# Optimization experiments

Measured on AMD Instinct MI355X. Metric: run time of the kernel, lower is better.

Reference implementation:

```python
import jax, jax.numpy as jnp
import numpy as np

B, T, D = 8, 1024, 768
N_HEAD = 12
HEAD_DIM = D // N_HEAD


def setup_inputs() -> dict:
    key = jax.random.key(0)
    k1, k2, k3, k4, k5 = jax.random.split(key, 5)
    x = jax.random.normal(k1, (B, T, D), dtype=jnp.float32)
    # c_attn: Linear(D, 3D); c_proj: Linear(D, D). Stored as (in, out) for x @ W.
    s_attn = 1.0 / np.sqrt(D)
    W_attn = jax.random.uniform(k2, (D, 3 * D), dtype=jnp.float32, minval=-s_attn, maxval=s_attn)
    b_attn = jax.random.uniform(k3, (3 * D,), dtype=jnp.float32, minval=-s_attn, maxval=s_attn)
    W_proj = jax.random.uniform(k4, (D, D), dtype=jnp.float32, minval=-s_attn, maxval=s_attn)
    b_proj = jax.random.uniform(k5, (D,), dtype=jnp.float32, minval=-s_attn, maxval=s_attn)
    return {"x": x, "W_attn": W_attn, "b_attn": b_attn, "W_proj": W_proj, "b_proj": b_proj}


def reference(x, W_attn, b_attn, W_proj, b_proj):
    Bs, Ts, Ds = x.shape
    qkv = x @ W_attn + b_attn  # [B, T, 3D]
    Q, K, V = jnp.split(qkv, 3, axis=2)
    # [B, H, T, hd]
    Q = Q.reshape(Bs, Ts, N_HEAD, HEAD_DIM).transpose(0, 2, 1, 3)
    K = K.reshape(Bs, Ts, N_HEAD, HEAD_DIM).transpose(0, 2, 1, 3)
    V = V.reshape(Bs, Ts, N_HEAD, HEAD_DIM).transpose(0, 2, 1, 3)
    scale = HEAD_DIM ** (-0.5)
    scores = jnp.einsum('bhqd,bhkd->bhqk', Q, K) * scale  # [B, H, T, T]
    causal = jnp.tril(jnp.ones((Ts, Ts), dtype=bool))
    scores = jnp.where(causal[None, None, :, :], scores, -jnp.inf)
    probs = jax.nn.softmax(scores, axis=-1)
    attn = jnp.einsum('bhqk,bhkd->bhqd', probs, V)  # [B, H, T, hd]
    attn = attn.transpose(0, 2, 1, 3).reshape(Bs, Ts, Ds)
    return attn @ W_proj + b_proj
```

## Files before the change

kernel.cpp:

```cpp
#include <hip/hip_runtime.h>
#include <hip/hip_bf16.h>

#define B_ 8
#define T_ 1024
#define D_ 768
#define NH 12
#define HD 64

typedef __bf16 bf16x8 __attribute__((ext_vector_type(8)));
typedef __bf16 bf16x4 __attribute__((ext_vector_type(4)));
typedef float f32x4 __attribute__((ext_vector_type(4)));
typedef short s16x4 __attribute__((ext_vector_type(4)));

__device__ __forceinline__ float fast_exp2(float x) {
  return __builtin_amdgcn_exp2f(x);
}

__device__ __forceinline__ f32x4 mfma32(bf16x8 a, bf16x8 b, f32x4 c) {
  return __builtin_amdgcn_mfma_f32_16x16x32_bf16(a, b, c, 0, 0, 0);
}

__device__ __forceinline__ f32x4 mfma16(bf16x4 a, bf16x4 b, f32x4 c) {
  union U { bf16x4 h; s16x4 s; };
  U ua; ua.h = a;
  U ub; ub.h = b;
  return __builtin_amdgcn_mfma_f32_16x16x16bf16_1k(ua.s, ub.s, c, 0, 0, 0);
}

__device__ __forceinline__ void gload_lds16(const void* g, void* l) {
  __builtin_amdgcn_global_load_lds((const __attribute__((address_space(1))) unsigned int*)g,
                                   (__attribute__((address_space(3))) unsigned int*)l, 16, 0, 0);
}

__global__ void xconv_kernel(const float* __restrict__ x, __bf16* __restrict__ xb, int n8) {
  int i = blockIdx.x * 256 + threadIdx.x;
  if (i >= n8) return;
  const float4* xf = (const float4*)x;
  float4 a = xf[i * 2], b = xf[i * 2 + 1];
  bf16x8 v;
  v[0] = (__bf16)a.x; v[1] = (__bf16)a.y; v[2] = (__bf16)a.z; v[3] = (__bf16)a.w;
  v[4] = (__bf16)b.x; v[5] = (__bf16)b.y; v[6] = (__bf16)b.z; v[7] = (__bf16)b.w;
  *(bf16x8*)&xb[(size_t)i * 8] = v;
}

__global__ void wtrans_kernel(const float* __restrict__ W, __bf16* __restrict__ WT, int K, int N) {
  __shared__ float tile[32][33];
  int t = threadIdx.x, col = t & 31, r0 = t >> 5;
  int n0 = blockIdx.x * 32, k0 = blockIdx.y * 32;
#pragma unroll
  for (int p = 0; p < 4; p++) {
    int r = r0 + p * 8;
    tile[r][col] = W[(size_t)(k0 + r) * N + n0 + col];
  }
  __syncthreads();
#pragma unroll
  for (int p = 0; p < 4; p++) {
    int r = r0 + p * 8;
    WT[(size_t)(n0 + r) * K + k0 + col] = (__bf16)tile[col][r];
  }
}

template <int EPI>
__global__ __launch_bounds__(256) void gemm_kernel(const __bf16* __restrict__ A,
                                                   const __bf16* __restrict__ BT,
                                                   const float* __restrict__ bias,
                                                   void* __restrict__ Cout,
                                                   __bf16* __restrict__ VT,
                                                   int M, int N, int K, int nbx) {
  __shared__ __align__(16) __bf16 Asm[2][128 * 64];
  __shared__ __align__(16) __bf16 Bsm[2][128 * 64];
  int tid = threadIdx.x;
  int wave = tid >> 6, lane = tid & 63, g = lane >> 4, l15 = lane & 15;
  int wr = wave >> 1, wc = wave & 1;

  int wg = blockIdx.x;
  int cpx = gridDim.x >> 3;
  int wg2 = (wg & 7) * cpx + (wg >> 3);
  int bx = wg2 % nbx, by = wg2 / nbx;
  int m0 = by * 128, n0 = bx * 128;

  int srow = tid >> 3;
  int cc = (tid & 7) ^ ((tid >> 3) & 7);
  const __bf16* Ag = A + (size_t)(m0 + srow) * K + cc * 8;
  const __bf16* Bg = BT + (size_t)(n0 + srow) * K + cc * 8;

  auto stage = [&](int kt, int bf) {
#pragma unroll
    for (int i = 0; i < 4; i++) {
      gload_lds16(Ag + (size_t)(i * 32) * K + kt * 64, &Asm[bf][wave * 512 + i * 2048]);
      gload_lds16(Bg + (size_t)(i * 32) * K + kt * 64, &Bsm[bf][wave * 512 + i * 2048]);
    }
  };

  f32x4 zz = {0.0f, 0.0f, 0.0f, 0.0f};
  f32x4 acc[4][4];
#pragma unroll
  for (int m = 0; m < 4; m++)
#pragma unroll
    for (int n = 0; n < 4; n++) acc[m][n] = zz;

  int nk = K >> 6;
  int swr = l15 & 7;

  stage(0, 0);

  int cur = 0;
  for (int kt = 0; kt < nk; kt++) {
    if (kt + 1 < nk) {
      stage(kt + 1, cur ^ 1);
      asm volatile("s_waitcnt vmcnt(8)" ::: "memory");
    } else {
      asm volatile("s_waitcnt vmcnt(0)" ::: "memory");
    }
    __builtin_amdgcn_s_barrier();
#pragma unroll
    for (int ks = 0; ks < 2; ks++) {
      bf16x8 af[4], bfr[4];
#pragma unroll
      for (int m = 0; m < 4; m++) {
        int row = wr * 64 + m * 16 + l15;
        af[m] = *(const bf16x8*)&Asm[cur][row * 64 + ((ks * 4 + g) ^ swr) * 8];
      }
#pragma unroll
      for (int n = 0; n < 4; n++) {
        int row = wc * 64 + n * 16 + l15;
        bfr[n] = *(const bf16x8*)&Bsm[cur][row * 64 + ((ks * 4 + g) ^ swr) * 8];
      }
#pragma unroll
      for (int m = 0; m < 4; m++)
#pragma unroll
        for (int n = 0; n < 4; n++)
          acc[m][n] = __builtin_amdgcn_mfma_f32_16x16x32_bf16(af[m], bfr[n], acc[m][n], 0, 0, 0);
    }
    asm volatile("" ::: "memory");
    __builtin_amdgcn_s_barrier();
    cur ^= 1;
  }
#pragma unroll
  for (int n = 0; n < 4; n++) {
    int gcol = n0 + wc * 64 + n * 16 + l15;
    float bv = bias[gcol];
#pragma unroll
    for (int m = 0; m < 4; m++) {
      int grow0 = m0 + wr * 64 + m * 16 + g * 4;
      float v0 = acc[m][n][0] + bv, v1 = acc[m][n][1] + bv;
      float v2 = acc[m][n][2] + bv, v3 = acc[m][n][3] + bv;
      if (EPI == 1) {
        float* C = (float*)Cout;
        C[(size_t)(grow0 + 0) * N + gcol] = v0;
        C[(size_t)(grow0 + 1) * N + gcol] = v1;
        C[(size_t)(grow0 + 2) * N + gcol] = v2;
        C[(size_t)(grow0 + 3) * N + gcol] = v3;
      } else if (gcol < 2 * D_) {
        __bf16* C = (__bf16*)Cout;
        C[(size_t)(grow0 + 0) * N + gcol] = (__bf16)v0;
        C[(size_t)(grow0 + 1) * N + gcol] = (__bf16)v1;
        C[(size_t)(grow0 + 2) * N + gcol] = (__bf16)v2;
        C[(size_t)(grow0 + 3) * N + gcol] = (__bf16)v3;
      } else {
        int hh = (gcol - 2 * D_) >> 6, dd = (gcol - 2 * D_) & 63;
        int bb = grow0 >> 10, tt = grow0 & 1023;
        bf16x4 sv = {(__bf16)v0, (__bf16)v1, (__bf16)v2, (__bf16)v3};
        *(bf16x4*)&VT[((size_t)(bb * NH + hh) * HD + dd) * T_ + tt] = sv;
      }
    }
  }
}

#define SCL 0.1803368801111204f

__global__ __launch_bounds__(256, 4) void attn_kernel(const __bf16* __restrict__ qkv,
                                                      const __bf16* __restrict__ VT,
                                                      __bf16* __restrict__ attn_out) {
  __shared__ __align__(16) __bf16 sm[2][2][4096];
  int tid = threadIdx.x;
  int wave = tid >> 6, lane = tid & 63, g = lane >> 4, l15 = lane & 15;
  int bh = blockIdx.x;
  int b = bh / NH, h = bh % NH;
  int qb = 15 - blockIdx.y;
  int q0w = qb * 64 + wave * 16;
  int nkt = qb + 1;
  int s0 = (bh + qb) % nkt;

  int kr = tid >> 3, cc = (tid & 7) ^ ((tid >> 3) & 7);
  const __bf16* Kst = qkv + (size_t)(b * T_ + kr) * (3 * D_) + D_ + h * HD + cc * 8;
  const __bf16* Vst = VT + ((size_t)bh * HD + kr) * T_ + cc * 8;
  __bf16* ldsK0 = &sm[0][0][wave * 512];
  __bf16* ldsV0 = &sm[0][1][wave * 512];
  __bf16* ldsK1 = &sm[1][0][wave * 512];
  __bf16* ldsV1 = &sm[1][1][wave * 512];

  auto stage = [&](int t, int bf) {
    size_t ko = (size_t)(t * 64) * (3 * D_);
    int vo = t * 64;
    __bf16* lk = bf ? ldsK1 : ldsK0;
    __bf16* lv = bf ? ldsV1 : ldsV0;
    gload_lds16(Kst + ko, lk);
    gload_lds16(Kst + ko + (size_t)32 * (3 * D_), lk + 2048);
    gload_lds16(Vst + vo, lv);
    gload_lds16(Vst + vo + 32 * T_, lv + 2048);
  };

  const __bf16* Qp = qkv + (size_t)(b * T_ + q0w + l15) * (3 * D_) + h * HD;
  bf16x8 qlo = *(const bf16x8*)(Qp + g * 8);
  bf16x8 qhi = *(const bf16x8*)(Qp + 32 + g * 8);

  f32x4 zz = {0.0f, 0.0f, 0.0f, 0.0f};
  f32x4 o0 = zz, o1 = zz, o2 = zz, o3 = zz;
  float m = -1e30f, l = 0.0f;
  int sw = l15 & 7;
  int clo = (g ^ sw) * 8;
  int chi = ((4 + g) ^ sw) * 8;

  stage(s0, 0);
  __syncthreads();

  int cur = 0;
  for (int i = 0; i < nkt; i++) {
    int kt = s0 + i;
    if (kt >= nkt) kt -= nkt;
    if (i + 1 < nkt) stage(kt + 1 == nkt ? 0 : kt + 1, cur ^ 1);

    const __bf16* Kb = &sm[cur][0][0];
    f32x4 s[4];
    __builtin_amdgcn_s_setprio(1);
#pragma unroll
    for (int kg = 0; kg < 4; kg++) {
      int rb = (kg * 16 + l15) * 64;
      bf16x8 kf = *(const bf16x8*)(Kb + rb + clo);
      bf16x8 kh = *(const bf16x8*)(Kb + rb + chi);
      s[kg] = mfma32(kf, qlo, zz);
      s[kg] = mfma32(kh, qhi, s[kg]);
    }
    __builtin_amdgcn_s_setprio(0);

    float v[16];
#pragma unroll
    for (int kg = 0; kg < 4; kg++)
#pragma unroll
      for (int r = 0; r < 4; r++) v[kg * 4 + r] = s[kg][r] * SCL;
    if (kt == qb) {
      int thr = wave * 16 + l15;
#pragma unroll
      for (int kg = 0; kg < 4; kg++)
#pragma unroll
        for (int r = 0; r < 4; r++)
          if (kg * 16 + g * 4 + r > thr) v[kg * 4 + r] = -1e30f;
    }
    float m0a = fmaxf(fmaxf(v[0], v[1]), fmaxf(v[2], v[3]));
    float m1a = fmaxf(fmaxf(v[4], v[5]), fmaxf(v[6], v[7]));
    float m2a = fmaxf(fmaxf(v[8], v[9]), fmaxf(v[10], v[11]));
    float m3a = fmaxf(fmaxf(v[12], v[13]), fmaxf(v[14], v[15]));
    float mx = fmaxf(fmaxf(m0a, m1a), fmaxf(m2a, m3a));
    mx = fmaxf(mx, __shfl_xor(mx, 16));
    mx = fmaxf(mx, __shfl_xor(mx, 32));
    if (!__all(mx <= m + 8.0f)) {
      float mnew = fmaxf(m, mx);
      float corr = fast_exp2(m - mnew);
      o0 *= corr; o1 *= corr; o2 *= corr; o3 *= corr;
      l *= corr;
      m = mnew;
    }
    float p[16], sum = 0.0f;
#pragma unroll
    for (int i2 = 0; i2 < 16; i2++) { p[i2] = fast_exp2(v[i2] - m); sum += p[i2]; }
    sum += __shfl_xor(sum, 16);
    sum += __shfl_xor(sum, 32);
    l += sum;
    bf16x4 pk[4];
#pragma unroll
    for (int kg = 0; kg < 4; kg++) {
      pk[kg][0] = (__bf16)p[kg * 4 + 0];
      pk[kg][1] = (__bf16)p[kg * 4 + 1];
      pk[kg][2] = (__bf16)p[kg * 4 + 2];
      pk[kg][3] = (__bf16)p[kg * 4 + 3];
    }

    const __bf16* Vb = &sm[cur][1][0];
    int vhalf = (g & 1) * 4;
    int vc = g >> 1;
    __builtin_amdgcn_s_setprio(1);
#pragma unroll
    for (int dq = 0; dq < 4; dq++) {
      int drow = (dq * 16 + l15) * 64;
#pragma unroll
      for (int ks = 0; ks < 4; ks++) {
        bf16x4 vf = *(const bf16x4*)(Vb + drow + ((ks * 2 + vc) ^ sw) * 8 + vhalf);
        f32x4* op = (dq == 0) ? &o0 : (dq == 1) ? &o1 : (dq == 2) ? &o2 : &o3;
        *op = mfma16(vf, pk[ks], *op);
      }
    }
    __builtin_amdgcn_s_setprio(0);

    __syncthreads();
    cur ^= 1;
  }

  float invl = 1.0f / l;
  __bf16* outp = attn_out + (size_t)(b * T_ + q0w + l15) * D_ + h * HD + g * 4;
  bf16x4 t0 = {(__bf16)(o0[0] * invl), (__bf16)(o0[1] * invl), (__bf16)(o0[2] * invl), (__bf16)(o0[3] * invl)};
  bf16x4 t1 = {(__bf16)(o1[0] * invl), (__bf16)(o1[1] * invl), (__bf16)(o1[2] * invl), (__bf16)(o1[3] * invl)};
  bf16x4 t2 = {(__bf16)(o2[0] * invl), (__bf16)(o2[1] * invl), (__bf16)(o2[2] * invl), (__bf16)(o2[3] * invl)};
  bf16x4 t3 = {(__bf16)(o3[0] * invl), (__bf16)(o3[1] * invl), (__bf16)(o3[2] * invl), (__bf16)(o3[3] * invl)};
  *(bf16x4*)(outp) = t0;
  *(bf16x4*)(outp + 16) = t1;
  *(bf16x4*)(outp + 32) = t2;
  *(bf16x4*)(outp + 48) = t3;
}

extern "C" void kernel_launch(void* const* d_in, const int* in_sizes, int n_in,
                              void* d_out, int out_size, void* d_ws, size_t ws_size,
                              hipStream_t stream) {
  (void)in_sizes; (void)n_in; (void)out_size; (void)ws_size;
  const float* x = (const float*)d_in[0];
  const float* W_attn = (const float*)d_in[1];
  const float* b_attn = (const float*)d_in[2];
  const float* W_proj = (const float*)d_in[3];
  const float* b_proj = (const float*)d_in[4];

  char* ws = (char*)d_ws;
  __bf16* xb  = (__bf16*)(ws + 0);
  __bf16* WaT = (__bf16*)(ws + 12582912);
  __bf16* WpT = (__bf16*)(ws + 16121856);
  __bf16* qkv = (__bf16*)(ws + 17301504);
  __bf16* VTb = (__bf16*)(ws + 55050240);
  __bf16* att = (__bf16*)(ws + 67633152);

  xconv_kernel<<<dim3(3072), 256, 0, stream>>>(x, xb, 786432);
  wtrans_kernel<<<dim3(72, 24), 256, 0, stream>>>(W_attn, WaT, 768, 2304);
  wtrans_kernel<<<dim3(24, 24), 256, 0, stream>>>(W_proj, WpT, 768, 768);
  gemm_kernel<0><<<dim3(1152), 256, 0, stream>>>(xb, WaT, b_attn, qkv, VTb, 8192, 2304, 768, 18);
  attn_kernel<<<dim3(96, 16), 256, 0, stream>>>(qkv, VTb, att);
  gemm_kernel<1><<<dim3(384), 256, 0, stream>>>(att, WpT, b_proj, d_out, nullptr, 8192, 768, 768, 6);
}
```

Measured before the change: 114.8 us.

## Use 256x128 tiles with 8 waves and split-stage pipelining for QKV GEMM

The QKV projection GEMM moves to a dedicated kernel with 512 threads and 256x128 output tiles, so each B tile in LDS is reused across twice as many rows. The global-to-LDS prefetch of the next K-tile is split into two halves interleaved with the two halves of the MFMA compute, and s_setprio raises wave priority during the math. The aim is less redundant B traffic and better overlap of loads with compute. The cost is a 96KB LDS footprint and half as many workgroups (576), which limits occupancy. The projection GEMM is split into its own non-templated kernel with unchanged logic.

```diff
diff --git a/kernel.cpp b/kernel.cpp
--- a/kernel.cpp
+++ b/kernel.cpp
@@ -31,6 +31,8 @@
   __builtin_amdgcn_global_load_lds((const __attribute__((address_space(1))) unsigned int*)g,
                                    (__attribute__((address_space(3))) unsigned int*)l, 16, 0, 0);
 }
+
+#define SBAR() asm volatile("s_barrier" ::: "memory")
 
 __global__ void xconv_kernel(const float* __restrict__ x, __bf16* __restrict__ xb, int n8) {
   int i = blockIdx.x * 256 + threadIdx.x;
@@ -60,13 +62,123 @@
   }
 }
 
-template <int EPI>
-__global__ __launch_bounds__(256) void gemm_kernel(const __bf16* __restrict__ A,
-                                                   const __bf16* __restrict__ BT,
-                                                   const float* __restrict__ bias,
-                                                   void* __restrict__ Cout,
-                                                   __bf16* __restrict__ VT,
-                                                   int M, int N, int K, int nbx) {
+__global__ __launch_bounds__(512) void gemm_qkv(const __bf16* __restrict__ A,
+                                                const __bf16* __restrict__ BT,
+                                                const float* __restrict__ bias,
+                                                __bf16* __restrict__ Cout,
+                                                __bf16* __restrict__ VT,
+                                                int M, int N, int K, int nbx) {
+  __shared__ __align__(16) __bf16 Asm[2][256 * 64];
+  __shared__ __align__(16) __bf16 Bsm[2][128 * 64];
+  int tid = threadIdx.x;
+  int wave = tid >> 6, lane = tid & 63, g = lane >> 4, l15 = lane & 15;
+  int wm = wave >> 1, wn = wave & 1;
+
+  int wg = blockIdx.x;
+  int cpx = gridDim.x >> 3;
+  int wg2 = (wg & 7) * cpx + (wg >> 3);
+  int bx = wg2 % nbx, by = wg2 / nbx;
+  int m0 = by * 256, n0 = bx * 128;
+
+  int srow = tid >> 3;
+  int cc = (tid & 7) ^ ((tid >> 3) & 7);
+  const __bf16* Ag = A + (size_t)(m0 + srow) * K + cc * 8;
+  const __bf16* Bg = BT + (size_t)(n0 + srow) * K + cc * 8;
+
+  auto stage_p1 = [&](int kt, int bf) {
+    gload_lds16(Ag + kt * 64, &Asm[bf][wave * 512]);
+    gload_lds16(Ag + (size_t)64 * K + kt * 64, &Asm[bf][4096 + wave * 512]);
+    gload_lds16(Bg + kt * 64, &Bsm[bf][wave * 512]);
+  };
+  auto stage_p2 = [&](int kt, int bf) {
+    gload_lds16(Ag + (size_t)128 * K + kt * 64, &Asm[bf][8192 + wave * 512]);
+    gload_lds16(Ag + (size_t)192 * K + kt * 64, &Asm[bf][12288 + wave * 512]);
+    gload_lds16(Bg + (size_t)64 * K + kt * 64, &Bsm[bf][4096 + wave * 512]);
+  };
+
+  f32x4 zz = {0.0f, 0.0f, 0.0f, 0.0f};
+  f32x4 acc[4][4];
+#pragma unroll
+  for (int m = 0; m < 4; m++)
+#pragma unroll
+    for (int n = 0; n < 4; n++) acc[m][n] = zz;
+
+  int nk = K >> 6;
+  int swr = l15 & 7;
+
+  auto compute_half = [&](int bf, int mh) {
+    __builtin_amdgcn_s_setprio(1);
+#pragma unroll
+    for (int ks = 0; ks < 2; ks++) {
+      bf16x8 af[2], bfr[4];
+#pragma unroll
+      for (int m2 = 0; m2 < 2; m2++) {
+        int row = wm * 64 + (mh * 2 + m2) * 16 + l15;
+        af[m2] = *(const bf16x8*)&Asm[bf][row * 64 + ((ks * 4 + g) ^ swr) * 8];
+      }
+#pragma unroll
+      for (int n = 0; n < 4; n++) {
+        int row = wn * 64 + n * 16 + l15;
+        bfr[n] = *(const bf16x8*)&Bsm[bf][row * 64 + ((ks * 4 + g) ^ swr) * 8];
+      }
+#pragma unroll
+      for (int m2 = 0; m2 < 2; m2++)
+#pragma unroll
+        for (int n = 0; n < 4; n++)
+          acc[mh * 2 + m2][n] =
+              __builtin_amdgcn_mfma_f32_16x16x32_bf16(af[m2], bfr[n], acc[mh * 2 + m2][n], 0, 0, 0);
+    }
+    __builtin_amdgcn_s_setprio(0);
+  };
+
+  stage_p1(0, 0);
+  stage_p2(0, 0);
+
+  for (int kt = 0; kt < nk; kt++) {
+    int bf = kt & 1, nbf = bf ^ 1;
+    if (kt + 1 < nk) {
+      stage_p1(kt + 1, nbf);
+      asm volatile("s_waitcnt vmcnt(3)" ::: "memory");
+    } else {
+      asm volatile("s_waitcnt vmcnt(0)" ::: "memory");
+    }
+    SBAR();
+    compute_half(bf, 0);
+    SBAR();
+    if (kt + 1 < nk) stage_p2(kt + 1, nbf);
+    compute_half(bf, 1);
+    SBAR();
+  }
+
+#pragma unroll
+  for (int n = 0; n < 4; n++) {
+    int gcol = n0 + wn * 64 + n * 16 + l15;
+    float bv = bias[gcol];
+#pragma unroll
+    for (int m = 0; m < 4; m++) {
+      int grow0 = m0 + wm * 64 + m * 16 + g * 4;
+      float v0 = acc[m][n][0] + bv, v1 = acc[m][n][1] + bv;
+      float v2 = acc[m][n][2] + bv, v3 = acc[m][n][3] + bv;
+      if (gcol < 2 * D_) {
+        Cout[(size_t)(grow0 + 0) * N + gcol] = (__bf16)v0;
+        Cout[(size_t)(grow0 + 1) * N + gcol] = (__bf16)v1;
+        Cout[(size_t)(grow0 + 2) * N + gcol] = (__bf16)v2;
+        Cout[(size_t)(grow0 + 3) * N + gcol] = (__bf16)v3;
+      } else {
+        int hh = (gcol - 2 * D_) >> 6, dd = (gcol - 2 * D_) & 63;
+        int bb = grow0 >> 10, tt = grow0 & 1023;
+        bf16x4 sv = {(__bf16)v0, (__bf16)v1, (__bf16)v2, (__bf16)v3};
+        *(bf16x4*)&VT[((size_t)(bb * NH + hh) * HD + dd) * T_ + tt] = sv;
+      }
+    }
+  }
+}
+
+__global__ __launch_bounds__(256) void gemm_proj(const __bf16* __restrict__ A,
+                                                 const __bf16* __restrict__ BT,
+                                                 const float* __restrict__ bias,
+                                                 float* __restrict__ Cout,
+                                                 int M, int N, int K, int nbx) {
   __shared__ __align__(16) __bf16 Asm[2][128 * 64];
   __shared__ __align__(16) __bf16 Bsm[2][128 * 64];
   int tid = threadIdx.x;
@@ -112,7 +224,7 @@
     } else {
       asm volatile("s_waitcnt vmcnt(0)" ::: "memory");
     }
-    __builtin_amdgcn_s_barrier();
+    SBAR();
 #pragma unroll
     for (int ks = 0; ks < 2; ks++) {
       bf16x8 af[4], bfr[4];
@@ -132,8 +244,7 @@
         for (int n = 0; n < 4; n++)
           acc[m][n] = __builtin_amdgcn_mfma_f32_16x16x32_bf16(af[m], bfr[n], acc[m][n], 0, 0, 0);
     }
-    asm volatile("" ::: "memory");
-    __builtin_amdgcn_s_barrier();
+    SBAR();
     cur ^= 1;
   }
 #pragma unroll
@@ -143,26 +254,9 @@
 #pragma unroll
     for (int m = 0; m < 4; m++) {
       int grow0 = m0 + wr * 64 + m * 16 + g * 4;
-      float v0 = acc[m][n][0] + bv, v1 = acc[m][n][1] + bv;
-      float v2 = acc[m][n][2] + bv, v3 = acc[m][n][3] + bv;
-      if (EPI == 1) {
-        float* C = (float*)Cout;
-        C[(size_t)(grow0 + 0) * N + gcol] = v0;
-        C[(size_t)(grow0 + 1) * N + gcol] = v1;
-        C[(size_t)(grow0 + 2) * N + gcol] = v2;
-        C[(size_t)(grow0 + 3) * N + gcol] = v3;
-      } else if (gcol < 2 * D_) {
-        __bf16* C = (__bf16*)Cout;
-        C[(size_t)(grow0 + 0) * N + gcol] = (__bf16)v0;
-        C[(size_t)(grow0 + 1) * N + gcol] = (__bf16)v1;
-        C[(size_t)(grow0 + 2) * N + gcol] = (__bf16)v2;
-        C[(size_t)(grow0 + 3) * N + gcol] = (__bf16)v3;
-      } else {
-        int hh = (gcol - 2 * D_) >> 6, dd = (gcol - 2 * D_) & 63;
-        int bb = grow0 >> 10, tt = grow0 & 1023;
-        bf16x4 sv = {(__bf16)v0, (__bf16)v1, (__bf16)v2, (__bf16)v3};
-        *(bf16x4*)&VT[((size_t)(bb * NH + hh) * HD + dd) * T_ + tt] = sv;
-      }
+#pragma unroll
+      for (int r = 0; r < 4; r++)
+        Cout[(size_t)(grow0 + r) * N + gcol] = acc[m][n][r] + bv;
     }
   }
 }
@@ -329,7 +423,7 @@
   xconv_kernel<<<dim3(3072), 256, 0, stream>>>(x, xb, 786432);
   wtrans_kernel<<<dim3(72, 24), 256, 0, stream>>>(W_attn, WaT, 768, 2304);
   wtrans_kernel<<<dim3(24, 24), 256, 0, stream>>>(W_proj, WpT, 768, 768);
-  gemm_kernel<0><<<dim3(1152), 256, 0, stream>>>(xb, WaT, b_attn, qkv, VTb, 8192, 2304, 768, 18);
+  gemm_qkv<<<dim3(576), 512, 0, stream>>>(xb, WaT, b_attn, qkv, VTb, 8192, 2304, 768, 18);
   attn_kernel<<<dim3(96, 16), 256, 0, stream>>>(qkv, VTb, att);
-  gemm_kernel<1><<<dim3(384), 256, 0, stream>>>(att, WpT, b_proj, d_out, nullptr, 8192, 768, 768, 6);
-}
+  gemm_proj<<<dim3(384), 256, 0, stream>>>(att, WpT, b_proj, (float*)d_out, 8192, 768, 768, 6);
+}
```

After: 135.7 us. 1.18x slower.
